# Optimization experiments

Measured on AMD Instinct MI355X. Metric: run time of the kernel, lower is better.

## Reference

```python
import jax, jax.numpy as jnp
import numpy as np

NUM_HEADS = 32
NUM_KV_HEADS = 8
HEAD_DIM = 128
PAGE_SIZE = 16
NUM_PAGES = 512
PAGES_PER_SEQ = 256  # 4096 cached tokens
Q_LEN = 1024
SCALE = 0.08838834764831845  # 1/sqrt(HEAD_DIM)


def setup_inputs() -> dict:
    key = jax.random.key(0)
    k1, k2, k3, k4, k5 = jax.random.split(key, 5)
    q = jax.random.normal(k1, (Q_LEN, NUM_HEADS * HEAD_DIM), dtype=jnp.float32)
    k = jax.random.normal(k2, (Q_LEN, NUM_KV_HEADS * HEAD_DIM), dtype=jnp.float32)
    v = jax.random.normal(k3, (Q_LEN, NUM_KV_HEADS * HEAD_DIM), dtype=jnp.float32)
    # paged KV cache: [num_pages, 2 (k/v), num_kv_heads, page_size, head_dim]
    kv_cache = jax.random.normal(
        k4, (NUM_PAGES, 2, NUM_KV_HEADS, PAGE_SIZE, HEAD_DIM), dtype=jnp.float32)
    block_table = jnp.sort(
        jax.random.randint(k5, (PAGES_PER_SEQ,), 0, NUM_PAGES, dtype=jnp.int32))
    return {"q": q, "k": k, "v": v, "kv_cache": kv_cache,
            "block_table": block_table}


def reference(q, k, v, kv_cache, block_table):
    # reshape flat projections into heads
    q = q.reshape(-1, NUM_HEADS, HEAD_DIM)          # [Tq, H, D]
    k = k.reshape(-1, NUM_KV_HEADS, HEAD_DIM)       # [Tq, Hkv, D]
    v = v.reshape(-1, NUM_KV_HEADS, HEAD_DIM)

    # gather paged KV cache into continuous tensors (all pages full)
    pages = kv_cache[block_table]                   # [P, 2, Hkv, ps, D]
    # per-page [Hkv, ps, D] -> [ps, Hkv, D], then concat along token dim
    past = jnp.transpose(pages, (1, 0, 3, 2, 4))    # [2, P, ps, Hkv, D]
    past = past.reshape(2, -1, NUM_KV_HEADS, HEAD_DIM)
    past_k, past_v = past[0], past[1]               # [Tpast, Hkv, D]

    k_full = jnp.concatenate([past_k, k], axis=0)   # [Tkv, Hkv, D]
    v_full = jnp.concatenate([past_v, v], axis=0)

    # GQA: repeat kv heads to match query heads
    heads_per_kv = NUM_HEADS // NUM_KV_HEADS
    k_full = jnp.repeat(k_full, heads_per_kv, axis=1)  # [Tkv, H, D]
    v_full = jnp.repeat(v_full, heads_per_kv, axis=1)

    qh = jnp.transpose(q, (1, 0, 2))                # [H, Tq, D]
    kh = jnp.transpose(k_full, (1, 0, 2))           # [H, Tkv, D]
    vh = jnp.transpose(v_full, (1, 0, 2))

    scores = jnp.einsum('hqd,hkd->hqk', qh, kh) * SCALE  # [H, Tq, Tkv]

    # prefill causal mask exactly as in the source: triu(ones(q_len, kv_len), 1)
    q_len, kv_len = qh.shape[1], kh.shape[1]
    causal = jnp.triu(jnp.ones((q_len, kv_len), dtype=bool), k=1)
    scores = jnp.where(causal[None, :, :], -jnp.inf, scores)

    attn = jax.nn.softmax(scores.astype(jnp.float32), axis=-1).astype(qh.dtype)
    out = jnp.einsum('hqk,hkd->hqd', attn, vh)      # [H, Tq, D]
    out = jnp.transpose(out, (1, 0, 2)).reshape(-1, NUM_HEADS * HEAD_DIM)
    return out
```

## Files before the change

### kernel.cpp

```cpp
#include <hip/hip_runtime.h>
#include <hip/hip_bf16.h>


#define NUM_HEADS 32
#define HEAD_DIM 128
#define Q_STRIDE 4096
#define SCALE 0.08838834764831845f
#define RESCALE_THR 8.0f
#define KSW_TILE 16384
#define VSW_OFF (2 * 1024 * 1024)

typedef short short8 __attribute__((ext_vector_type(8)));
typedef float f32x4 __attribute__((ext_vector_type(4)));
typedef unsigned short ushort_t;
typedef unsigned int uint_t;

__device__ __forceinline__ ushort_t f2bf(float f) {
    return __builtin_bit_cast(ushort_t, __float2bfloat16(f));
}
__device__ __forceinline__ uint_t pk2(float a, float b) {
    return (uint_t)f2bf(a) | ((uint_t)f2bf(b) << 16);
}

__launch_bounds__(256)
__global__ void prep_kv(const float* __restrict__ kvc,
                        const int* __restrict__ bt,
                        char* __restrict__ wsb)
{
    __shared__ float sVt[64 * 128];
    const int blk = blockIdx.x;
    const int hkv = blk >> 4;
    const int jb  = blk & 15;
    const int tid = threadIdx.x;
    char* kout = wsb + (size_t)(hkv * 16 + jb) * KSW_TILE;
    char* vout = wsb + VSW_OFF + (size_t)(hkv * 16 + jb) * KSW_TILE;

#pragma unroll
    for (int i = 0; i < 4; ++i) {
        const int u = tid + i * 256;
        const int t = u >> 4, c = u & 15;
        const int gtok = jb * 64 + t;
        const int page = bt[gtok >> 4];
        const float* src = kvc + (size_t)page * 32768 + (size_t)hkv * 2048
                         + (gtok & 15) * 128 + c * 8;
        float4 a = *(const float4*)src;
        float4 b = *(const float4*)(src + 4);
        uint4 p;
        p.x = pk2(a.x, a.y); p.y = pk2(a.z, a.w);
        p.z = pk2(b.x, b.y); p.w = pk2(b.z, b.w);
        *(uint4*)(kout + t * 256 + ((c * 16) ^ ((t & 7) << 4))) = p;
    }
#pragma unroll
    for (int i = 0; i < 8; ++i) {
        const int u = tid + i * 256;
        const int t = u >> 5, c4 = u & 31;
        const int gtok = jb * 64 + t;
        const int page = bt[gtok >> 4];
        const float* src = kvc + (size_t)page * 32768 + 16384
                         + (size_t)hkv * 2048 + (gtok & 15) * 128 + c4 * 4;
        *(float4*)(sVt + t * 128 + c4 * 4) = *(const float4*)src;
    }
    __syncthreads();
#pragma unroll
    for (int i = 0; i < 4; ++i) {
        const int u = tid + i * 256;
        const int d = u >> 3, ch = u & 7;
        float v[8];
#pragma unroll
        for (int k = 0; k < 8; ++k) v[k] = sVt[(8 * ch + k) * 128 + d];
        uint4 p;
        p.x = pk2(v[0], v[1]); p.y = pk2(v[2], v[3]);
        p.z = pk2(v[4], v[5]); p.w = pk2(v[6], v[7]);
        *(uint4*)(vout + ((d * 128 + 16 * ch) ^ ((d & 7) << 4))) = p;
    }
}

#define GLL16(G, L) __builtin_amdgcn_global_load_lds(                         \
    (const uint_t __attribute__((address_space(1)))*)(G),                     \
    (uint_t __attribute__((address_space(3)))*)(L), 16, 0, 0)

#define STAGE(JB, KB, VB) {                                                   \
    const char* ks = kvbf + (size_t)(hkv * 16 + (JB)) * KSW_TILE              \
                   + w * 4096 + lane * 16;                                    \
    const char* vs = ks + VSW_OFF;                                            \
    _Pragma("unroll")                                                         \
    for (int i = 0; i < 4; ++i) {                                             \
        GLL16(ks + i * 1024, (KB) + w * 4096 + i * 1024);                     \
        GLL16(vs + i * 1024, (VB) + w * 4096 + i * 1024);                     \
    }                                                                         \
}

__launch_bounds__(256)
__global__ void attn_main(const float* __restrict__ q,
                          const char* __restrict__ kvbf,
                          float* __restrict__ out)
{
    __shared__ __align__(16) char sK[2][16384];
    __shared__ __align__(16) char sV[2][16384];
    __shared__ __align__(16) char sP[4][2048];

    const int bid = blockIdx.x;
    const int h   = bid & 31;
    const int qt  = 15 - (bid >> 5);
    const int hkv = h >> 2;
    const int tid  = threadIdx.x;
    const int w    = tid >> 6;
    const int lane = tid & 63;
    const int l15  = lane & 15;
    const int lhi  = lane >> 4;

    short8 qf[4];
    {
        const int qrow = qt * 64 + w * 16 + l15;
        const float* qp = q + (size_t)qrow * Q_STRIDE + h * HEAD_DIM;
#pragma unroll
        for (int s = 0; s < 4; ++s) {
            const int d0 = s * 32 + lhi * 8;
            float4 a = *(const float4*)(qp + d0);
            float4 b = *(const float4*)(qp + d0 + 4);
            short8 v;
            v[0] = (short)f2bf(a.x * SCALE); v[1] = (short)f2bf(a.y * SCALE);
            v[2] = (short)f2bf(a.z * SCALE); v[3] = (short)f2bf(a.w * SCALE);
            v[4] = (short)f2bf(b.x * SCALE); v[5] = (short)f2bf(b.y * SCALE);
            v[6] = (short)f2bf(b.z * SCALE); v[7] = (short)f2bf(b.w * SCALE);
            qf[s] = v;
        }
    }

    f32x4 acc[8];
#pragma unroll
    for (int n2 = 0; n2 < 8; ++n2) acc[n2] = (f32x4){0.f, 0.f, 0.f, 0.f};
    float m_run[4]  = {-1e30f, -1e30f, -1e30f, -1e30f};
    float l_part[4] = {0.f, 0.f, 0.f, 0.f};

    STAGE(0, sK[0], sV[0])
    __syncthreads();

    for (int jb = 0; jb <= qt; ++jb) {
        const int cur = jb & 1;
        char* kbuf = sK[cur];
        char* vbuf = sV[cur];
        const bool pf = (jb < qt);
        if (pf) {
            STAGE(jb + 1, sK[cur ^ 1], sV[cur ^ 1])
            asm volatile("s_waitcnt vmcnt(8)" ::: "memory");
        } else {
            asm volatile("s_waitcnt vmcnt(0)" ::: "memory");
        }
        __builtin_amdgcn_sched_barrier(0);
        __builtin_amdgcn_s_barrier();
        __builtin_amdgcn_sched_barrier(0);

        f32x4 sacc[4];
#pragma unroll
        for (int n = 0; n < 4; ++n) sacc[n] = (f32x4){0.f, 0.f, 0.f, 0.f};
#pragma unroll
        for (int s = 0; s < 4; ++s) {
#pragma unroll
            for (int n = 0; n < 4; ++n) {
                const int tok = n * 16 + l15;
                const uint_t byte = (uint_t)(tok * 256)
                    + (((uint_t)((s * 32 + lhi * 8) * 2)) ^ ((uint_t)((tok & 7) << 4)));
                short8 kb = *(const short8*)(kbuf + byte);
                sacc[n] = __builtin_amdgcn_mfma_f32_16x16x32_bf16(qf[s], kb, sacc[n], 0, 0, 0);
            }
        }

        const bool diag = (jb == qt);
        float pv[4][4];
#pragma unroll
        for (int n = 0; n < 4; ++n)
#pragma unroll
            for (int j = 0; j < 4; ++j) {
                float x = sacc[n][j];
                if (diag) {
                    const int tok = jb * 64 + n * 16 + l15;
                    const int qg  = qt * 64 + w * 16 + lhi * 4 + j;
                    if (tok > qg) x = -1e30f;
                }
                pv[n][j] = x;
            }
#pragma unroll
        for (int j = 0; j < 4; ++j) {
            float lmax = fmaxf(fmaxf(pv[0][j], pv[1][j]), fmaxf(pv[2][j], pv[3][j]));
            if (__any(lmax > m_run[j] + RESCALE_THR)) {
                float mt = lmax;
#pragma unroll
                for (int off = 1; off < 16; off <<= 1)
                    mt = fmaxf(mt, __shfl_xor(mt, off));
                const float mn = fmaxf(m_run[j], mt);
                const float alpha = __expf(m_run[j] - mn);
                m_run[j] = mn;
                l_part[j] *= alpha;
#pragma unroll
                for (int n2 = 0; n2 < 8; ++n2) acc[n2][j] *= alpha;
            }
            float ls = 0.f;
#pragma unroll
            for (int n = 0; n < 4; ++n) {
                float p = __expf(pv[n][j] - m_run[j]);
                pv[n][j] = p;
                ls += p;
            }
            l_part[j] += ls;
        }

        char* pb = sP[w];
#pragma unroll
        for (int n = 0; n < 4; ++n)
#pragma unroll
            for (int j = 0; j < 4; ++j) {
                const int r = lhi * 4 + j;
                const uint_t byte = (uint_t)(r * 128)
                    + (((uint_t)((n * 16 + l15) * 2)) ^ ((uint_t)((r & 7) << 4)));
                *(ushort_t*)(pb + byte) = f2bf(pv[n][j]);
            }

#pragma unroll
        for (int s2 = 0; s2 < 2; ++s2) {
            const uint_t pbyte = (uint_t)(l15 * 128)
                + (((uint_t)((s2 * 32 + lhi * 8) * 2)) ^ ((uint_t)((l15 & 7) << 4)));
            short8 pa = *(const short8*)(pb + pbyte);
#pragma unroll
            for (int n2 = 0; n2 < 8; ++n2) {
                const int dim = n2 * 16 + l15;
                const uint_t vbyte = (uint_t)(dim * 128)
                    + (((uint_t)((s2 * 32 + lhi * 8) * 2)) ^ ((uint_t)((dim & 7) << 4)));
                short8 vbf = *(const short8*)(vbuf + vbyte);
                acc[n2] = __builtin_amdgcn_mfma_f32_16x16x32_bf16(pa, vbf, acc[n2], 0, 0, 0);
            }
        }

        if (pf) {
            __builtin_amdgcn_sched_barrier(0);
            __builtin_amdgcn_s_barrier();
        }
    }

#pragma unroll
    for (int j = 0; j < 4; ++j) {
        float lsum = l_part[j];
#pragma unroll
        for (int off = 1; off < 16; off <<= 1)
            lsum += __shfl_xor(lsum, off);
        const float inv = 1.0f / lsum;
        const int qg = qt * 64 + w * 16 + lhi * 4 + j;
        float* dst = out + (size_t)qg * Q_STRIDE + h * HEAD_DIM;
#pragma unroll
        for (int n2 = 0; n2 < 8; ++n2)
            dst[n2 * 16 + l15] = acc[n2][j] * inv;
    }
}

extern "C" void kernel_launch(void* const* d_in, const int* in_sizes, int n_in,
                              void* d_out, int out_size, void* d_ws, size_t ws_size,
                              hipStream_t stream) {
    const float* q   = (const float*)d_in[0];
    const float* kvc = (const float*)d_in[3];
    const int*   bt  = (const int*)d_in[4];
    float* out = (float*)d_out;
    char*  wsb = (char*)d_ws;
    prep_kv<<<dim3(128), dim3(256), 0, stream>>>(kvc, bt, wsb);
    attn_main<<<dim3(512), dim3(256), 0, stream>>>(q, wsb, out);
}
```

Baseline: 45.75 us.

## Defer PV MFMAs to next iteration, use exp2 with log2e-folded scale, set priority

The P·V matrix multiply for each KV block is moved into the next iteration. The P and V fragments are loaded into registers at the end of one iteration and consumed at the start of the next, alongside the QK MFMAs, so the softmax VALU/exp work can overlap with matrix work. The query scale now folds in log2(e), so exp2f replaces __expf, and s_setprio raises wave priority around the MFMA section. The cost is higher register pressure from holding 16 V fragments plus two P fragments, which may hurt occupancy or cause spills.

Measured after the change: 44.74 us. -2.2%, faster.

```diff
diff --git a/kernel.cpp b/kernel.cpp
--- a/kernel.cpp
+++ b/kernel.cpp
@@ -5,7 +5,7 @@
 #define NUM_HEADS 32
 #define HEAD_DIM 128
 #define Q_STRIDE 4096
-#define SCALE 0.08838834764831845f
+#define SCALE2 0.1275179114285314f
 #define RESCALE_THR 8.0f
 #define KSW_TILE 16384
 #define VSW_OFF (2 * 1024 * 1024)
@@ -119,10 +119,10 @@
             float4 a = *(const float4*)(qp + d0);
             float4 b = *(const float4*)(qp + d0 + 4);
             short8 v;
-            v[0] = (short)f2bf(a.x * SCALE); v[1] = (short)f2bf(a.y * SCALE);
-            v[2] = (short)f2bf(a.z * SCALE); v[3] = (short)f2bf(a.w * SCALE);
-            v[4] = (short)f2bf(b.x * SCALE); v[5] = (short)f2bf(b.y * SCALE);
-            v[6] = (short)f2bf(b.z * SCALE); v[7] = (short)f2bf(b.w * SCALE);
+            v[0] = (short)f2bf(a.x * SCALE2); v[1] = (short)f2bf(a.y * SCALE2);
+            v[2] = (short)f2bf(a.z * SCALE2); v[3] = (short)f2bf(a.w * SCALE2);
+            v[4] = (short)f2bf(b.x * SCALE2); v[5] = (short)f2bf(b.y * SCALE2);
+            v[6] = (short)f2bf(b.z * SCALE2); v[7] = (short)f2bf(b.w * SCALE2);
             qf[s] = v;
         }
     }
@@ -133,9 +133,13 @@
     float m_run[4]  = {-1e30f, -1e30f, -1e30f, -1e30f};
     float l_part[4] = {0.f, 0.f, 0.f, 0.f};
 
+    short8 pap0, pap1;
+    short8 vbp[2][8];
+
     STAGE(0, sK[0], sV[0])
     __syncthreads();
 
+    char* pb = sP[w];
     for (int jb = 0; jb <= qt; ++jb) {
         const int cur = jb & 1;
         char* kbuf = sK[cur];
@@ -151,6 +155,15 @@
         __builtin_amdgcn_s_barrier();
         __builtin_amdgcn_sched_barrier(0);
 
+        __builtin_amdgcn_s_setprio(1);
+        if (jb > 0) {
+#pragma unroll
+            for (int n2 = 0; n2 < 8; ++n2) {
+                acc[n2] = __builtin_amdgcn_mfma_f32_16x16x32_bf16(pap0, vbp[0][n2], acc[n2], 0, 0, 0);
+                acc[n2] = __builtin_amdgcn_mfma_f32_16x16x32_bf16(pap1, vbp[1][n2], acc[n2], 0, 0, 0);
+            }
+        }
+
         f32x4 sacc[4];
 #pragma unroll
         for (int n = 0; n < 4; ++n) sacc[n] = (f32x4){0.f, 0.f, 0.f, 0.f};
@@ -165,31 +178,30 @@
                 sacc[n] = __builtin_amdgcn_mfma_f32_16x16x32_bf16(qf[s], kb, sacc[n], 0, 0, 0);
             }
         }
+        __builtin_amdgcn_s_setprio(0);
 
         const bool diag = (jb == qt);
-        float pv[4][4];
-#pragma unroll
-        for (int n = 0; n < 4; ++n)
-#pragma unroll
-            for (int j = 0; j < 4; ++j) {
-                float x = sacc[n][j];
-                if (diag) {
+        if (diag) {
+#pragma unroll
+            for (int n = 0; n < 4; ++n)
+#pragma unroll
+                for (int j = 0; j < 4; ++j) {
                     const int tok = jb * 64 + n * 16 + l15;
                     const int qg  = qt * 64 + w * 16 + lhi * 4 + j;
-                    if (tok > qg) x = -1e30f;
+                    if (tok > qg) sacc[n][j] = -1e30f;
                 }
-                pv[n][j] = x;
-            }
+        }
 #pragma unroll
         for (int j = 0; j < 4; ++j) {
-            float lmax = fmaxf(fmaxf(pv[0][j], pv[1][j]), fmaxf(pv[2][j], pv[3][j]));
+            float lmax = fmaxf(fmaxf(sacc[0][j], sacc[1][j]),
+                               fmaxf(sacc[2][j], sacc[3][j]));
             if (__any(lmax > m_run[j] + RESCALE_THR)) {
                 float mt = lmax;
 #pragma unroll
                 for (int off = 1; off < 16; off <<= 1)
                     mt = fmaxf(mt, __shfl_xor(mt, off));
                 const float mn = fmaxf(m_run[j], mt);
-                const float alpha = __expf(m_run[j] - mn);
+                const float alpha = exp2f(m_run[j] - mn);
                 m_run[j] = mn;
                 l_part[j] *= alpha;
 #pragma unroll
@@ -198,14 +210,13 @@
             float ls = 0.f;
 #pragma unroll
             for (int n = 0; n < 4; ++n) {
-                float p = __expf(pv[n][j] - m_run[j]);
-                pv[n][j] = p;
+                float p = exp2f(sacc[n][j] - m_run[j]);
+                sacc[n][j] = p;
                 ls += p;
             }
             l_part[j] += ls;
         }
 
-        char* pb = sP[w];
 #pragma unroll
         for (int n = 0; n < 4; ++n)
 #pragma unroll
@@ -213,28 +224,41 @@
                 const int r = lhi * 4 + j;
                 const uint_t byte = (uint_t)(r * 128)
                     + (((uint_t)((n * 16 + l15) * 2)) ^ ((uint_t)((r & 7) << 4)));
-                *(ushort_t*)(pb + byte) = f2bf(pv[n][j]);
-            }
-
-#pragma unroll
-        for (int s2 = 0; s2 < 2; ++s2) {
-            const uint_t pbyte = (uint_t)(l15 * 128)
-                + (((uint_t)((s2 * 32 + lhi * 8) * 2)) ^ ((uint_t)((l15 & 7) << 4)));
-            short8 pa = *(const short8*)(pb + pbyte);
+                *(ushort_t*)(pb + byte) = f2bf(sacc[n][j]);
+            }
+
+        {
+            const uint_t pbyte0 = (uint_t)(l15 * 128)
+                + (((uint_t)((lhi * 8) * 2)) ^ ((uint_t)((l15 & 7) << 4)));
+            pap0 = *(const short8*)(pb + pbyte0);
+            const uint_t pbyte1 = (uint_t)(l15 * 128)
+                + (((uint_t)((32 + lhi * 8) * 2)) ^ ((uint_t)((l15 & 7) << 4)));
+            pap1 = *(const short8*)(pb + pbyte1);
+        }
+#pragma unroll
+        for (int s2 = 0; s2 < 2; ++s2)
 #pragma unroll
             for (int n2 = 0; n2 < 8; ++n2) {
                 const int dim = n2 * 16 + l15;
                 const uint_t vbyte = (uint_t)(dim * 128)
                     + (((uint_t)((s2 * 32 + lhi * 8) * 2)) ^ ((uint_t)((dim & 7) << 4)));
-                short8 vbf = *(const short8*)(vbuf + vbyte);
-                acc[n2] = __builtin_amdgcn_mfma_f32_16x16x32_bf16(pa, vbf, acc[n2], 0, 0, 0);
-            }
-        }
+                vbp[s2][n2] = *(const short8*)(vbuf + vbyte);
+            }
 
         if (pf) {
+            asm volatile("s_waitcnt lgkmcnt(0)" ::: "memory");
             __builtin_amdgcn_sched_barrier(0);
             __builtin_amdgcn_s_barrier();
-        }
+            __builtin_amdgcn_sched_barrier(0);
+        }
+    }
+
+    asm volatile("s_waitcnt lgkmcnt(0)" ::: "memory");
+    __builtin_amdgcn_sched_barrier(0);
+#pragma unroll
+    for (int n2 = 0; n2 < 8; ++n2) {
+        acc[n2] = __builtin_amdgcn_mfma_f32_16x16x32_bf16(pap0, vbp[0][n2], acc[n2], 0, 0, 0);
+        acc[n2] = __builtin_amdgcn_mfma_f32_16x16x32_bf16(pap1, vbp[1][n2], acc[n2], 0, 0, 0);
     }
 
 #pragma unroll
```
